# Kernel optimization log

Measured on AMD Instinct MI355X. Metric: run time of the kernel, lower is better.

## Reference

```python
import jax, jax.numpy as jnp
import numpy as np

HIDDEN = 512


def _lstm(x, kernel, rec, bias):
    # x: [B,T,D]; Keras gate order i,f,c(g),o
    xz = jnp.einsum('btd,dk->btk', x, kernel) + bias  # [B,T,4H]
    B = x.shape[0]
    init = (jnp.zeros((B, HIDDEN), x.dtype), jnp.zeros((B, HIDDEN), x.dtype))

    def step(carry, z_t):
        h, c = carry
        z = z_t + h @ rec
        i, f, g, o = jnp.split(z, 4, axis=-1)
        c = jax.nn.sigmoid(f) * c + jax.nn.sigmoid(i) * jnp.tanh(g)
        h = jax.nn.sigmoid(o) * jnp.tanh(c)
        return (h, c), h

    _, hs = jax.lax.scan(step, init, jnp.swapaxes(xz, 0, 1))
    return jnp.swapaxes(hs, 0, 1)  # [B,T,H]


def _bilstm(x, kf, rf, bf, kb, rb, bb):
    fwd = _lstm(x, kf, rf, bf)
    bwd = _lstm(x[:, ::-1], kb, rb, bb)[:, ::-1]
    return jnp.concatenate([fwd, bwd], axis=-1)  # [B,T,2H]


def _crf_nll(logits, tags, seq_lens, trans):
    # logits [B,T,N], tags [B,T] int, seq_lens [B] int, trans [N,N]
    B, T, N = logits.shape
    t_idx = jnp.arange(T)
    mask = (t_idx[None, :] < seq_lens[:, None])  # [B,T] bool
    maskf = mask.astype(logits.dtype)

    # gold sequence score: unary + pairwise transitions
    unary = jnp.take_along_axis(logits, tags[..., None], axis=-1)[..., 0]  # [B,T]
    unary_score = jnp.sum(unary * maskf, axis=-1)
    pair_maskf = maskf[:, 1:]  # pair (t-1,t) valid iff t < len
    binary = trans[tags[:, :-1], tags[:, 1:]]  # [B,T-1]
    binary_score = jnp.sum(binary * pair_maskf, axis=-1)

    # log-partition via forward algorithm (masked scan)
    alpha0 = logits[:, 0]  # [B,N]

    def step(alpha, inp):
        logit_t, valid = inp
        new = jax.nn.logsumexp(alpha[:, :, None] + trans[None], axis=1) + logit_t
        return jnp.where(valid[:, None], new, alpha), None

    xs = (jnp.swapaxes(logits[:, 1:], 0, 1), jnp.swapaxes(mask[:, 1:], 0, 1))
    alpha, _ = jax.lax.scan(step, alpha0, xs)
    log_z = jax.nn.logsumexp(alpha, axis=-1)  # [B]
    return -(unary_score + binary_score - log_z)


def setup_inputs() -> dict:
    key = jax.random.key(0)
    ks = jax.random.split(key, 12)
    B, T, D, H, N = 32, 256, 768, HIDDEN, 25
    s_in = 1.0 / np.sqrt(D)
    s_rec = 1.0 / np.sqrt(H)
    return {
        'embeddings': jax.random.normal(ks[0], (B, T, D), jnp.float32),
        'targets': jax.random.randint(ks[1], (B, T), 0, N, jnp.int32),
        'seq_lens': jax.random.randint(ks[2], (B,), 1, T + 1, jnp.int32),
        'k_fwd': jax.random.normal(ks[3], (D, 4 * H), jnp.float32) * s_in,
        'r_fwd': jax.random.normal(ks[4], (H, 4 * H), jnp.float32) * s_rec,
        'b_fwd': jnp.zeros((4 * H,), jnp.float32),
        'k_bwd': jax.random.normal(ks[5], (D, 4 * H), jnp.float32) * s_in,
        'r_bwd': jax.random.normal(ks[6], (H, 4 * H), jnp.float32) * s_rec,
        'b_bwd': jnp.zeros((4 * H,), jnp.float32),
        'dense_w': jax.random.normal(ks[7], (2 * H, N), jnp.float32) / np.sqrt(2 * H),
        'dense_b': jnp.zeros((N,), jnp.float32),
        'transitions': jax.random.uniform(ks[8], (N, N), jnp.float32),
    }


def reference(embeddings, targets, seq_lens, k_fwd, r_fwd, b_fwd,
              k_bwd, r_bwd, b_bwd, dense_w, dense_b, transitions):
    seq_lens = jnp.clip(seq_lens, 1, embeddings.shape[1])
    h = _bilstm(embeddings, k_fwd, r_fwd, b_fwd, k_bwd, r_bwd, b_bwd)
    logits = jax.nn.selu(jnp.einsum('bth,hn->btn', h, dense_w) + dense_b)
    nll = _crf_nll(logits, targets, seq_lens, transitions)  # [B]
    loss = jnp.mean(nll)
    return loss, logits
```

## Files before the change

kernel.cpp:

```cpp
#include <hip/hip_runtime.h>
#include <hip/hip_bf16.h>
#include <math.h>

#define HID 512
#define GATES 2048
#define BT 8192
#define TT 256
#define BB 32
#define DIN 768
#define NTAG 25
#define UPB 4
#define NBLK 128
#define FSTR 4
#define EREP 8
#define ESTR 16

typedef _Float16 half2v __attribute__((ext_vector_type(2)));
typedef _Float16 half8  __attribute__((ext_vector_type(8)));
typedef float    f32x4  __attribute__((ext_vector_type(4)));

__device__ __forceinline__ half2v pack2h(float a, float b) {
  return __builtin_bit_cast(half2v, __builtin_amdgcn_cvt_pkrtz(a, b));
}

__device__ __forceinline__ float sigf(float x) { return 1.f / (1.f + __expf(-x)); }

__device__ __forceinline__ void gld_lds16(const void* g, void* l) {
  __builtin_amdgcn_global_load_lds(
      (const __attribute__((address_space(1))) unsigned int*)g,
      (__attribute__((address_space(3))) unsigned int*)l, 16, 0, 0);
}

__global__ __launch_bounds__(256) void convert_emb(
    const float* __restrict__ emb, unsigned short* __restrict__ emb16)
{
  const int m = blockIdx.x * 8 + (threadIdx.x >> 5);
  const int c0 = threadIdx.x & 31;
  #pragma unroll
  for (int p = 0; p < 3; ++p) {
    const int c = c0 + p * 32;
    const int kb = c >> 3, s = c & 7;
    const float* src = emb + (size_t)m * DIN + c * 8;
    const float4 v0 = *(const float4*)src;
    const float4 v1 = *(const float4*)(src + 4);
    half8 hv;
    hv[0] = (_Float16)v0.x; hv[1] = (_Float16)v0.y;
    hv[2] = (_Float16)v0.z; hv[3] = (_Float16)v0.w;
    hv[4] = (_Float16)v1.x; hv[5] = (_Float16)v1.y;
    hv[6] = (_Float16)v1.z; hv[7] = (_Float16)v1.w;
    *(half8*)(emb16 + (size_t)m * DIN + kb * 64 + (s ^ (m & 7)) * 8) = hv;
  }
}

__global__ __launch_bounds__(256) void transpose_k(
    const float* __restrict__ Kf, const float* __restrict__ Kb,
    unsigned short* __restrict__ KTf, unsigned short* __restrict__ KTb)
{
  const int dir = blockIdx.z;
  const float* __restrict__ K = dir ? Kb : Kf;
  unsigned short* __restrict__ KT = dir ? KTb : KTf;
  const int k0 = blockIdx.x * 64;
  const int n0 = blockIdx.y * 64;
  __shared__ float tile[64][65];
  const int tid = threadIdx.x;
  #pragma unroll
  for (int p = 0; p < 4; ++p) {
    const int idx = p * 256 + tid;
    const int kr = idx >> 4, c4 = (idx & 15) * 4;
    const float4 v = *(const float4*)(K + (size_t)(k0 + kr) * GATES + n0 + c4);
    tile[kr][c4 + 0] = v.x; tile[kr][c4 + 1] = v.y;
    tile[kr][c4 + 2] = v.z; tile[kr][c4 + 3] = v.w;
  }
  __syncthreads();
  #pragma unroll
  for (int p = 0; p < 2; ++p) {
    const int idx = p * 256 + tid;
    const int nr = idx >> 3, s = idx & 7;
    half8 hv;
    #pragma unroll
    for (int x = 0; x < 8; ++x) hv[x] = (_Float16)tile[s * 8 + x][nr];
    *(half8*)(KT + (size_t)(n0 + nr) * DIN + k0 + (s ^ (nr & 7)) * 8) = hv;
  }
}

__global__ __launch_bounds__(256) void prep_w(
    const float* __restrict__ W, unsigned short* __restrict__ WT16)
{
  for (int id = threadIdx.x; id < 32 * 1024; id += 256) {
    const int n = id >> 10, k = id & 1023;
    const float v = (n < NTAG) ? W[(size_t)k * NTAG + n] : 0.f;
    ((_Float16*)WT16)[id] = (_Float16)v;
  }
}

__global__ __launch_bounds__(256) void gemm_xz(
    const unsigned short* __restrict__ emb16,
    const unsigned short* __restrict__ KTf, const unsigned short* __restrict__ KTb,
    const float* __restrict__ bf, const float* __restrict__ bb,
    float* __restrict__ xzf, float* __restrict__ xzb)
{
  const int dir = blockIdx.z;
  const unsigned short* __restrict__ KT = dir ? KTb : KTf;
  const float* __restrict__ bias = dir ? bb : bf;
  float* __restrict__ C = dir ? xzb : xzf;
  const int n0 = blockIdx.x * 128;
  const int m0 = blockIdx.y * 128;

  __shared__ __align__(16) char A_lds[128 * 64 * 2];
  __shared__ __align__(16) char B_lds[128 * 64 * 2];

  const int tid = threadIdx.x;
  const int lane = tid & 63, wid = tid >> 6;
  const int wm = wid >> 1, wn = wid & 1;
  const int lm = lane & 15, lk = lane >> 4;

  f32x4 acc[4][4];
  #pragma unroll
  for (int i = 0; i < 4; ++i)
    #pragma unroll
    for (int j = 0; j < 4; ++j) acc[i][j] = (f32x4){0.f, 0.f, 0.f, 0.f};

  for (int kt = 0; kt < DIN / 64; ++kt) {
    __syncthreads();
    #pragma unroll
    for (int i = 0; i < 4; ++i) {
      const int g = wid * 256 + i * 64 + lane;
      const int r = g >> 3, s = g & 7;
      gld_lds16(emb16 + (size_t)(m0 + r) * DIN + (kt * 8 + s) * 8,
                A_lds + (size_t)(wid * 256 + i * 64) * 16);
      gld_lds16(KT + (size_t)(n0 + r) * DIN + (kt * 8 + s) * 8,
                B_lds + (size_t)(wid * 256 + i * 64) * 16);
    }
    __syncthreads();

    #pragma unroll
    for (int kh = 0; kh < 2; ++kh) {
      half8 a[4], b[4];
      #pragma unroll
      for (int mt = 0; mt < 4; ++mt) {
        const int rloc = wm * 64 + mt * 16 + lm;
        const int kslot = kh * 4 + lk;
        a[mt] = *(const half8*)(A_lds + rloc * 128 + ((kslot ^ (rloc & 7)) << 4));
      }
      #pragma unroll
      for (int nt = 0; nt < 4; ++nt) {
        const int nloc = wn * 64 + nt * 16 + lm;
        const int kslot = kh * 4 + lk;
        b[nt] = *(const half8*)(B_lds + nloc * 128 + ((kslot ^ (nloc & 7)) << 4));
      }
      #pragma unroll
      for (int mt = 0; mt < 4; ++mt)
        #pragma unroll
        for (int nt = 0; nt < 4; ++nt)
          acc[mt][nt] = __builtin_amdgcn_mfma_f32_16x16x32_f16(a[mt], b[nt], acc[mt][nt], 0, 0, 0);
    }
  }

  #pragma unroll
  for (int nt = 0; nt < 4; ++nt) {
    const int col = n0 + wn * 64 + nt * 16 + lm;
    const float bs = bias[col];
    #pragma unroll
    for (int mt = 0; mt < 4; ++mt) {
      const int rowb = m0 + wm * 64 + mt * 16 + lk * 4;
      const f32x4 v = acc[mt][nt];
      #pragma unroll
      for (int g = 0; g < 4; ++g)
        C[(size_t)(rowb + g) * GATES + col] = v[g] + bs;
    }
  }
}

__global__ __launch_bounds__(256, 1) void lstm_persist(
    const float* __restrict__ xzf, const float* __restrict__ xzb,
    const float* __restrict__ Rf, const float* __restrict__ Rb,
    unsigned int* __restrict__ hGf, unsigned int* __restrict__ hGb,
    int* __restrict__ flg,
    int* __restrict__ ep)
{
  const int bid = blockIdx.x;
  const int dir = bid & 1;
  const int blk = bid >> 1;
  const int u0 = blk * UPB;
  const int tid = threadIdx.x;
  const int c = tid & 15;
  const int j = (c & 3) * HID + u0 + (c >> 2);
  const int lane = tid & 63, w = tid >> 6;
  const int lm = lane & 15, lk = lane >> 4;

  const float* __restrict__ R  = dir ? Rb : Rf;
  const float* __restrict__ xz = dir ? xzb : xzf;
  unsigned int* __restrict__ hGd = dir ? hGb : hGf;
  int* __restrict__ flgd = flg + (size_t)dir * TT * NBLK * FSTR;
  int* __restrict__ epd  = ep  + (size_t)dir * TT * EREP * ESTR;

  __shared__ uint4 hs4[BB * 65];
  __shared__ float redm[4][BB][18];
  __shared__ float zbuf[BB][20];

  half8 Rbf[4];
  #pragma unroll
  for (int kti = 0; kti < 4; ++kti) {
    const int kb = (w * 4 + kti) * 32 + lk * 8;
    half8 hv;
    #pragma unroll
    for (int x = 0; x < 8; ++x) hv[x] = (_Float16)R[(size_t)(kb + x) * GATES + j];
    Rbf[kti] = hv;
  }

  float cst = 0.f;
  const int b_o = tid & 31, u_o = tid >> 5;
  const int fb0 = tid >> 4, fb1 = (tid >> 4) + 16;
  const bool leader = (blk == 0);

  for (int s = 0; s < TT; ++s) {
    const int t = dir ? (TT - 1 - s) : s;

    const float x0 = xz[((size_t)fb0 * TT + t) * GATES + j];
    const float x1 = xz[((size_t)fb1 * TT + t) * GATES + j];

    if (s > 0) {
      const int tprev = dir ? t + 1 : t - 1;
      if (leader) {
        if (tid < NBLK) {
          while (!__hip_atomic_load(&flgd[((s - 1) * NBLK + tid) * FSTR],
                                    __ATOMIC_RELAXED, __HIP_MEMORY_SCOPE_AGENT))
            __builtin_amdgcn_s_sleep(1);
        }
        __syncthreads();
        if (tid < EREP)
          __hip_atomic_store(&epd[((s - 1) * EREP + tid) * ESTR], 1,
                             __ATOMIC_RELAXED, __HIP_MEMORY_SCOPE_AGENT);
      } else {
        if (tid == 0) {
          while (!__hip_atomic_load(&epd[((s - 1) * EREP + (blk & 7)) * ESTR],
                                    __ATOMIC_RELAXED, __HIP_MEMORY_SCOPE_AGENT))
            __builtin_amdgcn_s_sleep(1);
        }
        __syncthreads();
      }
      const uint4* hsrc = (const uint4*)(hGd + (size_t)tprev * BB * 256);
      #pragma unroll
      for (int it = 0; it < 8; ++it) {
        const int g4 = tid + it * 256;
        const uint4 v = hsrc[g4];
        hs4[(g4 >> 6) * 65 + (g4 & 63)] = v;
      }
    } else {
      const uint4 zz = make_uint4(0u, 0u, 0u, 0u);
      #pragma unroll
      for (int it = 0; it < 9; ++it) {
        const int idx = tid + it * 256;
        if (idx < BB * 65) hs4[idx] = zz;
      }
    }
    __syncthreads();

    f32x4 acc0 = (f32x4){0.f, 0.f, 0.f, 0.f};
    f32x4 acc1 = (f32x4){0.f, 0.f, 0.f, 0.f};
    #pragma unroll
    for (int kti = 0; kti < 4; ++kti) {
      const int k4 = (w * 4 + kti) * 4 + lk;
      const half8 a0 = *(const half8*)&hs4[(lm) * 65 + k4];
      const half8 a1 = *(const half8*)&hs4[(16 + lm) * 65 + k4];
      acc0 = __builtin_amdgcn_mfma_f32_16x16x32_f16(a0, Rbf[kti], acc0, 0, 0, 0);
      acc1 = __builtin_amdgcn_mfma_f32_16x16x32_f16(a1, Rbf[kti], acc1, 0, 0, 0);
    }
    #pragma unroll
    for (int g = 0; g < 4; ++g) {
      redm[w][lk * 4 + g][lm] = acc0[g];
      redm[w][16 + lk * 4 + g][lm] = acc1[g];
    }
    __syncthreads();

    {
      const float za = redm[0][fb0][c] + redm[1][fb0][c] + redm[2][fb0][c] + redm[3][fb0][c] + x0;
      const float zb2 = redm[0][fb1][c] + redm[1][fb1][c] + redm[2][fb1][c] + redm[3][fb1][c] + x1;
      zbuf[fb0][c] = za;
      zbuf[fb1][c] = zb2;
    }
    __syncthreads();

    if (tid < 128) {
      const float zi = zbuf[b_o][u_o * 4 + 0];
      const float zf = zbuf[b_o][u_o * 4 + 1];
      const float zg = zbuf[b_o][u_o * 4 + 2];
      const float zo = zbuf[b_o][u_o * 4 + 3];
      cst = sigf(zf) * cst + sigf(zi) * tanhf(zg);
      const float h = sigf(zo) * tanhf(cst);
      const float hp2 = __shfl_xor(h, 32);
      if ((tid & 32) == 0) {
        const half2v p = pack2h(h, hp2);
        __hip_atomic_store(&hGd[((size_t)t * BB + b_o) * 256 + blk * 2 + (u_o >> 1)],
                           __builtin_bit_cast(unsigned int, p),
                           __ATOMIC_RELAXED, __HIP_MEMORY_SCOPE_AGENT);
      }
    }
    __syncthreads();
    if (tid == 0)
      __hip_atomic_store(&flgd[(s * NBLK + blk) * FSTR], 1, __ATOMIC_RELAXED,
                         __HIP_MEMORY_SCOPE_AGENT);
  }
}

__global__ __launch_bounds__(256) void dense_selu(
    const unsigned int* __restrict__ hGf, const unsigned int* __restrict__ hGb,
    const unsigned short* __restrict__ WT16, const float* __restrict__ bias,
    float* __restrict__ out)
{
  const int q0 = blockIdx.x * 128;
  __shared__ __align__(16) char A_lds[128 * 64 * 2];
  __shared__ __align__(16) char B_lds[32 * 64 * 2];

  const int tid = threadIdx.x;
  const int lane = tid & 63, w = tid >> 6;
  const int lm = lane & 15, lk = lane >> 4;

  f32x4 acc[2][2];
  #pragma unroll
  for (int i = 0; i < 2; ++i)
    #pragma unroll
    for (int jj = 0; jj < 2; ++jj) acc[i][jj] = (f32x4){0.f, 0.f, 0.f, 0.f};

  for (int kt = 0; kt < 16; ++kt) {
    const int k0 = kt * 64;
    __syncthreads();
    #pragma unroll
    for (int p = 0; p < 4; ++p) {
      const int id = p * 256 + tid;
      const int r = id >> 3, s = id & 7;
      const int k = k0 + s * 8;
      const unsigned int* src = (k < 512)
          ? hGf + (size_t)(q0 + r) * 256 + (k >> 1)
          : hGb + (size_t)(q0 + r) * 256 + ((k - 512) >> 1);
      const uint4 v = *(const uint4*)src;
      *(uint4*)(A_lds + r * 128 + ((s ^ (r & 7)) << 4)) = v;
    }
    {
      const int r = tid >> 3, s = tid & 7;
      const uint4 v = *(const uint4*)(WT16 + (size_t)r * 1024 + k0 + s * 8);
      *(uint4*)(B_lds + r * 128 + ((s ^ (r & 7)) << 4)) = v;
    }
    __syncthreads();

    #pragma unroll
    for (int kh = 0; kh < 2; ++kh) {
      const int kslot = kh * 4 + lk;
      half8 a[2], b[2];
      #pragma unroll
      for (int mt = 0; mt < 2; ++mt) {
        const int rloc = w * 32 + mt * 16 + lm;
        a[mt] = *(const half8*)(A_lds + rloc * 128 + ((kslot ^ (rloc & 7)) << 4));
      }
      #pragma unroll
      for (int nt = 0; nt < 2; ++nt) {
        const int nloc = nt * 16 + lm;
        b[nt] = *(const half8*)(B_lds + nloc * 128 + ((kslot ^ (nloc & 7)) << 4));
      }
      #pragma unroll
      for (int mt = 0; mt < 2; ++mt)
        #pragma unroll
        for (int nt = 0; nt < 2; ++nt)
          acc[mt][nt] = __builtin_amdgcn_mfma_f32_16x16x32_f16(a[mt], b[nt], acc[mt][nt], 0, 0, 0);
    }
  }

  const float scale = 1.0507009873554805f, alf = 1.6732632423543772f;
  #pragma unroll
  for (int nt = 0; nt < 2; ++nt) {
    const int col = nt * 16 + lm;
    if (col < NTAG) {
      const float bs = bias[col];
      #pragma unroll
      for (int mt = 0; mt < 2; ++mt) {
        const int rowb = q0 + w * 32 + mt * 16 + lk * 4;
        const f32x4 vv = acc[mt][nt];
        #pragma unroll
        for (int g = 0; g < 4; ++g) {
          const int q = rowb + g;
          const int bt = (q & 31) * 256 + (q >> 5);
          float v = vv[g] + bs;
          v = v > 0.f ? scale * v : scale * alf * (__expf(v) - 1.f);
          out[(size_t)bt * NTAG + col] = v;
        }
      }
    }
  }
}

__global__ __launch_bounds__(64) void crf_kernel(
    const float* __restrict__ logits,
    const int* __restrict__ tags, const int* __restrict__ lens,
    const float* __restrict__ trans, float* __restrict__ nll)
{
  const int b = blockIdx.x;
  const int tid = threadIdx.x;
  __shared__ float tr[NTAG * NTAG];
  __shared__ float al[NTAG];
  __shared__ float red[2];
  for (int i = tid; i < NTAG * NTAG; i += 64) tr[i] = trans[i];
  __syncthreads();

  int len = lens[b];
  len = len < 1 ? 1 : (len > TT ? TT : len);
  const size_t base = (size_t)b * TT;

  float us = 0.f, bs = 0.f;
  for (int t = tid; t < TT; t += 64) {
    if (t < len) us += logits[(base + t) * NTAG + tags[base + t]];
    if (t >= 1 && t < len) bs += tr[tags[base + t - 1] * NTAG + tags[base + t]];
  }
  #pragma unroll
  for (int off = 32; off > 0; off >>= 1) {
    us += __shfl_down(us, off);
    bs += __shfl_down(bs, off);
  }
  if (tid == 0) { red[0] = us; red[1] = bs; }

  if (tid < NTAG) al[tid] = logits[base * NTAG + tid];
  __syncthreads();

  for (int t = 1; t < len; ++t) {
    float nv = 0.f;
    if (tid < NTAG) {
      float m = -3.4e38f;
      #pragma unroll
      for (int i = 0; i < NTAG; ++i) m = fmaxf(m, al[i] + tr[i * NTAG + tid]);
      float ss = 0.f;
      #pragma unroll
      for (int i = 0; i < NTAG; ++i) ss += __expf(al[i] + tr[i * NTAG + tid] - m);
      nv = m + __logf(ss) + logits[(base + t) * NTAG + tid];
    }
    __syncthreads();
    if (tid < NTAG) al[tid] = nv;
    __syncthreads();
  }

  if (tid == 0) {
    float m = -3.4e38f;
    for (int i = 0; i < NTAG; ++i) m = fmaxf(m, al[i]);
    float ss = 0.f;
    for (int i = 0; i < NTAG; ++i) ss += __expf(al[i] - m);
    const float logz = m + __logf(ss);
    nll[b] = -(red[0] + red[1] - logz);
  }
}

__global__ __launch_bounds__(64) void finalize(const float* __restrict__ nll, float* __restrict__ out) {
  float v = (threadIdx.x < BB) ? nll[threadIdx.x] : 0.f;
  #pragma unroll
  for (int off = 32; off > 0; off >>= 1) v += __shfl_down(v, off);
  if (threadIdx.x == 0) out[0] = v * (1.f / BB);
}

extern "C" void kernel_launch(void* const* d_in, const int* in_sizes, int n_in,
                              void* d_out, int out_size, void* d_ws, size_t ws_size,
                              hipStream_t stream) {
  const float* emb  = (const float*)d_in[0];
  const int* tags   = (const int*)d_in[1];
  const int* lens   = (const int*)d_in[2];
  const float* kf   = (const float*)d_in[3];
  const float* rf   = (const float*)d_in[4];
  const float* bf   = (const float*)d_in[5];
  const float* kb   = (const float*)d_in[6];
  const float* rb   = (const float*)d_in[7];
  const float* bb   = (const float*)d_in[8];
  const float* dw   = (const float*)d_in[9];
  const float* db   = (const float*)d_in[10];
  const float* trans= (const float*)d_in[11];
  float* out = (float*)d_out;

  float* ws  = (float*)d_ws;
  float* xzf = ws;
  float* xzb = xzf + (size_t)BT * GATES;
  unsigned int* hGf = (unsigned int*)(xzb + (size_t)BT * GATES);
  unsigned int* hGb = hGf + (size_t)TT * BB * 256;
  unsigned short* emb16 = (unsigned short*)(hGb + (size_t)TT * BB * 256);
  unsigned short* KTf = emb16 + (size_t)BT * DIN;
  unsigned short* KTb = KTf + (size_t)GATES * DIN;
  unsigned short* WT16 = KTb + (size_t)GATES * DIN;
  float* nll = (float*)(WT16 + 32 * 1024);
  int*   flg = (int*)(nll + 64);
  int*   ep  = flg + 2 * TT * NBLK * FSTR;

  (void)hipMemsetAsync(flg, 0,
                       (size_t)(2 * TT * NBLK * FSTR + 2 * TT * EREP * ESTR) * 4,
                       stream);

  convert_emb<<<BT / 8, 256, 0, stream>>>(emb, emb16);
  transpose_k<<<dim3(DIN / 64, GATES / 64, 2), 256, 0, stream>>>(kf, kb, KTf, KTb);
  prep_w<<<1, 256, 0, stream>>>(dw, WT16);
  gemm_xz<<<dim3(GATES / 128, BT / 128, 2), 256, 0, stream>>>(emb16, KTf, KTb, bf, bb, xzf, xzb);
  lstm_persist<<<2 * NBLK, 256, 0, stream>>>(xzf, xzb, rf, rb, hGf, hGb, flg, ep);
  dense_selu<<<BT / 128, 256, 0, stream>>>(hGf, hGb, WT16, db, out + 1);
  crf_kernel<<<32, 64, 0, stream>>>(out + 1, tags, lens, trans, nll);
  finalize<<<1, 64, 0, stream>>>(nll, out);
}
```

Measured before the change: 973.0 us.

## Load recurrent h operands straight from global and merge prep kernels

```diff
diff --git a/kernel.cpp b/kernel.cpp
--- a/kernel.cpp
+++ b/kernel.cpp
@@ -31,65 +31,65 @@
       (__attribute__((address_space(3))) unsigned int*)l, 16, 0, 0);
 }
 
-__global__ __launch_bounds__(256) void convert_emb(
-    const float* __restrict__ emb, unsigned short* __restrict__ emb16)
-{
-  const int m = blockIdx.x * 8 + (threadIdx.x >> 5);
-  const int c0 = threadIdx.x & 31;
-  #pragma unroll
-  for (int p = 0; p < 3; ++p) {
-    const int c = c0 + p * 32;
-    const int kb = c >> 3, s = c & 7;
-    const float* src = emb + (size_t)m * DIN + c * 8;
-    const float4 v0 = *(const float4*)src;
-    const float4 v1 = *(const float4*)(src + 4);
-    half8 hv;
-    hv[0] = (_Float16)v0.x; hv[1] = (_Float16)v0.y;
-    hv[2] = (_Float16)v0.z; hv[3] = (_Float16)v0.w;
-    hv[4] = (_Float16)v1.x; hv[5] = (_Float16)v1.y;
-    hv[6] = (_Float16)v1.z; hv[7] = (_Float16)v1.w;
-    *(half8*)(emb16 + (size_t)m * DIN + kb * 64 + (s ^ (m & 7)) * 8) = hv;
-  }
-}
-
-__global__ __launch_bounds__(256) void transpose_k(
+__global__ __launch_bounds__(256) void prep_all(
+    const float* __restrict__ emb, unsigned short* __restrict__ emb16,
     const float* __restrict__ Kf, const float* __restrict__ Kb,
-    unsigned short* __restrict__ KTf, unsigned short* __restrict__ KTb)
-{
-  const int dir = blockIdx.z;
-  const float* __restrict__ K = dir ? Kb : Kf;
-  unsigned short* __restrict__ KT = dir ? KTb : KTf;
-  const int k0 = blockIdx.x * 64;
-  const int n0 = blockIdx.y * 64;
-  __shared__ float tile[64][65];
-  const int tid = threadIdx.x;
-  #pragma unroll
-  for (int p = 0; p < 4; ++p) {
-    const int idx = p * 256 + tid;
-    const int kr = idx >> 4, c4 = (idx & 15) * 4;
-    const float4 v = *(const float4*)(K + (size_t)(k0 + kr) * GATES + n0 + c4);
-    tile[kr][c4 + 0] = v.x; tile[kr][c4 + 1] = v.y;
-    tile[kr][c4 + 2] = v.z; tile[kr][c4 + 3] = v.w;
-  }
-  __syncthreads();
-  #pragma unroll
-  for (int p = 0; p < 2; ++p) {
-    const int idx = p * 256 + tid;
-    const int nr = idx >> 3, s = idx & 7;
-    half8 hv;
-    #pragma unroll
-    for (int x = 0; x < 8; ++x) hv[x] = (_Float16)tile[s * 8 + x][nr];
-    *(half8*)(KT + (size_t)(n0 + nr) * DIN + k0 + (s ^ (nr & 7)) * 8) = hv;
-  }
-}
-
-__global__ __launch_bounds__(256) void prep_w(
+    unsigned short* __restrict__ KTf, unsigned short* __restrict__ KTb,
     const float* __restrict__ W, unsigned short* __restrict__ WT16)
 {
-  for (int id = threadIdx.x; id < 32 * 1024; id += 256) {
-    const int n = id >> 10, k = id & 1023;
-    const float v = (n < NTAG) ? W[(size_t)k * NTAG + n] : 0.f;
-    ((_Float16*)WT16)[id] = (_Float16)v;
+  __shared__ float tile[64][65];
+  const int bid = blockIdx.x;
+  const int tid = threadIdx.x;
+
+  if (bid < 1024) {
+    const int m = bid * 8 + (tid >> 5);
+    const int c0 = tid & 31;
+    #pragma unroll
+    for (int p = 0; p < 3; ++p) {
+      const int c = c0 + p * 32;
+      const int kb = c >> 3, s = c & 7;
+      const float* src = emb + (size_t)m * DIN + c * 8;
+      const float4 v0 = *(const float4*)src;
+      const float4 v1 = *(const float4*)(src + 4);
+      half8 hv;
+      hv[0] = (_Float16)v0.x; hv[1] = (_Float16)v0.y;
+      hv[2] = (_Float16)v0.z; hv[3] = (_Float16)v0.w;
+      hv[4] = (_Float16)v1.x; hv[5] = (_Float16)v1.y;
+      hv[6] = (_Float16)v1.z; hv[7] = (_Float16)v1.w;
+      *(half8*)(emb16 + (size_t)m * DIN + kb * 64 + (s ^ (m & 7)) * 8) = hv;
+    }
+  } else if (bid < 1792) {
+    const int r = bid - 1024;
+    const int dir = r / 384;
+    const int r2 = r % 384;
+    const int k0 = (r2 >> 5) * 64;
+    const int n0 = (r2 & 31) * 64;
+    const float* __restrict__ K = dir ? Kb : Kf;
+    unsigned short* __restrict__ KT = dir ? KTb : KTf;
+    #pragma unroll
+    for (int p = 0; p < 4; ++p) {
+      const int idx = p * 256 + tid;
+      const int kr = idx >> 4, c4 = (idx & 15) * 4;
+      const float4 v = *(const float4*)(K + (size_t)(k0 + kr) * GATES + n0 + c4);
+      tile[kr][c4 + 0] = v.x; tile[kr][c4 + 1] = v.y;
+      tile[kr][c4 + 2] = v.z; tile[kr][c4 + 3] = v.w;
+    }
+    __syncthreads();
+    #pragma unroll
+    for (int p = 0; p < 2; ++p) {
+      const int idx = p * 256 + tid;
+      const int nr = idx >> 3, s = idx & 7;
+      half8 hv;
+      #pragma unroll
+      for (int x = 0; x < 8; ++x) hv[x] = (_Float16)tile[s * 8 + x][nr];
+      *(half8*)(KT + (size_t)(n0 + nr) * DIN + k0 + (s ^ (nr & 7)) * 8) = hv;
+    }
+  } else {
+    for (int id = tid; id < 32 * 1024; id += 256) {
+      const int n = id >> 10, k = id & 1023;
+      const float v = (n < NTAG) ? W[(size_t)k * NTAG + n] : 0.f;
+      ((_Float16*)WT16)[id] = (_Float16)v;
+    }
   }
 }
 
@@ -194,7 +194,6 @@
   int* __restrict__ flgd = flg + (size_t)dir * TT * NBLK * FSTR;
   int* __restrict__ epd  = ep  + (size_t)dir * TT * EREP * ESTR;
 
-  __shared__ uint4 hs4[BB * 65];
   __shared__ float redm[4][BB][18];
   __shared__ float zbuf[BB][20];
 
@@ -218,6 +217,9 @@
 
     const float x0 = xz[((size_t)fb0 * TT + t) * GATES + j];
     const float x1 = xz[((size_t)fb1 * TT + t) * GATES + j];
+
+    f32x4 acc0 = (f32x4){0.f, 0.f, 0.f, 0.f};
+    f32x4 acc1 = (f32x4){0.f, 0.f, 0.f, 0.f};
 
     if (s > 0) {
       const int tprev = dir ? t + 1 : t - 1;
@@ -239,33 +241,23 @@
         }
         __syncthreads();
       }
-      const uint4* hsrc = (const uint4*)(hGd + (size_t)tprev * BB * 256);
-      #pragma unroll
-      for (int it = 0; it < 8; ++it) {
-        const int g4 = tid + it * 256;
-        const uint4 v = hsrc[g4];
-        hs4[(g4 >> 6) * 65 + (g4 & 63)] = v;
-      }
-    } else {
-      const uint4 zz = make_uint4(0u, 0u, 0u, 0u);
-      #pragma unroll
-      for (int it = 0; it < 9; ++it) {
-        const int idx = tid + it * 256;
-        if (idx < BB * 65) hs4[idx] = zz;
-      }
-    }
-    __syncthreads();
-
-    f32x4 acc0 = (f32x4){0.f, 0.f, 0.f, 0.f};
-    f32x4 acc1 = (f32x4){0.f, 0.f, 0.f, 0.f};
-    #pragma unroll
-    for (int kti = 0; kti < 4; ++kti) {
-      const int k4 = (w * 4 + kti) * 4 + lk;
-      const half8 a0 = *(const half8*)&hs4[(lm) * 65 + k4];
-      const half8 a1 = *(const half8*)&hs4[(16 + lm) * 65 + k4];
-      acc0 = __builtin_amdgcn_mfma_f32_16x16x32_f16(a0, Rbf[kti], acc0, 0, 0, 0);
-      acc1 = __builtin_amdgcn_mfma_f32_16x16x32_f16(a1, Rbf[kti], acc1, 0, 0, 0);
-    }
+      const uint4* hrow = (const uint4*)(hGd + (size_t)tprev * BB * 256);
+      uint4 a0[4], a1[4];
+      #pragma unroll
+      for (int kti = 0; kti < 4; ++kti) {
+        const int k4 = (w * 4 + kti) * 4 + lk;
+        a0[kti] = hrow[lm * 64 + k4];
+        a1[kti] = hrow[(16 + lm) * 64 + k4];
+      }
+      #pragma unroll
+      for (int kti = 0; kti < 4; ++kti) {
+        acc0 = __builtin_amdgcn_mfma_f32_16x16x32_f16(
+            __builtin_bit_cast(half8, a0[kti]), Rbf[kti], acc0, 0, 0, 0);
+        acc1 = __builtin_amdgcn_mfma_f32_16x16x32_f16(
+            __builtin_bit_cast(half8, a1[kti]), Rbf[kti], acc1, 0, 0, 0);
+      }
+    }
+
     #pragma unroll
     for (int g = 0; g < 4; ++g) {
       redm[w][lk * 4 + g][lm] = acc0[g];
@@ -487,9 +479,7 @@
                        (size_t)(2 * TT * NBLK * FSTR + 2 * TT * EREP * ESTR) * 4,
                        stream);
 
-  convert_emb<<<BT / 8, 256, 0, stream>>>(emb, emb16);
-  transpose_k<<<dim3(DIN / 64, GATES / 64, 2), 256, 0, stream>>>(kf, kb, KTf, KTb);
-  prep_w<<<1, 256, 0, stream>>>(dw, WT16);
+  prep_all<<<1793, 256, 0, stream>>>(emb, emb16, kf, kb, KTf, KTb, dw, WT16);
   gemm_xz<<<dim3(GATES / 128, BT / 128, 2), 256, 0, stream>>>(emb16, KTf, KTb, bf, bb, xzf, xzb);
   lstm_persist<<<2 * NBLK, 256, 0, stream>>>(xzf, xzb, rf, rb, hGf, hGb, flg, ep);
   dense_selu<<<BT / 128, 256, 0, stream>>>(hGf, hGb, WT16, db, out + 1);
```

Measured after the change: 1.205 ms. 1.24x slower.
